# Optimization experiments

Hardware: AMD Instinct MI355X
Metric: run time of the kernel (lower is better)

## Reference

```python
import jax, jax.numpy as jnp
import numpy as np

D_MODEL = 1024
NUM_HEADS = 16
D_STATE = D_MODEL // NUM_HEADS
BS, SEQ = 8, 1024
NEG_BIG = 1e10


def setup_inputs() -> dict:
    key = jax.random.key(0)
    ks = jax.random.split(key, 3)
    std = 0.02
    x = jax.random.normal(ks[0], (BS, SEQ, D_MODEL), dtype=jnp.float32)
    qkv_w = jax.random.normal(ks[1], (D_MODEL, 3 * D_MODEL), dtype=jnp.float32) * std
    qkv_b = jnp.zeros((3 * D_MODEL,), dtype=jnp.float32)
    out_w = jax.random.normal(ks[2], (D_MODEL, D_MODEL), dtype=jnp.float32) * std
    out_b = jnp.zeros((D_MODEL,), dtype=jnp.float32)
    return {"x": x, "qkv_w": qkv_w, "qkv_b": qkv_b, "out_w": out_w, "out_b": out_b}


def reference(x, qkv_w, qkv_b, out_w, out_b):
    bs, n, d = x.shape
    qkv = jnp.matmul(x, qkv_w) + qkv_b  # [bs, n, 3*d_model]
    q, k, v = jnp.split(qkv, 3, axis=-1)

    def split_heads(t):  # [bs, n, d] -> [bs, h, n, d_state]
        return t.reshape(bs, n, NUM_HEADS, D_STATE).transpose(0, 2, 1, 3)

    q, k, v = split_heads(q), split_heads(k), split_heads(v)
    scale = 1.0 / np.sqrt(D_STATE).astype(np.float32)
    scores = jnp.einsum('bhqd,bhkd->bhqk', q, k) * scale  # [bs,h,n,n]
    # causal mask: i >= j (mask(n) with ns==nd)
    m = (jnp.arange(n)[:, None] >= jnp.arange(n)[None, :]).astype(scores.dtype)
    scores = scores * m - (1.0 - m) * NEG_BIG
    attn = jax.nn.softmax(scores, axis=-1)
    out = jnp.einsum('bhqk,bhkd->bhqd', attn, v)  # [bs,h,n,d_state]
    out = out.transpose(0, 2, 1, 3).reshape(bs, n, d)
    return jnp.matmul(out, out_w) + out_b
```

## Files before the change

kernel.cpp:

```cpp
#include <hip/hip_runtime.h>
#include <hip/hip_bf16.h>
#include <stdint.h>

typedef __attribute__((ext_vector_type(8))) __bf16 bf16x8;
typedef __attribute__((ext_vector_type(4))) float f32x4;
typedef __attribute__((ext_vector_type(4))) unsigned int u32x4;
typedef __attribute__((ext_vector_type(4))) unsigned short u16x4;

#define SEQ 1024
#define DM 1024

#if __has_builtin(__builtin_amdgcn_exp2f)
#define EXP2(x) __builtin_amdgcn_exp2f(x)
#else
#define EXP2(x) exp2f(x)
#endif

typedef __attribute__((address_space(3))) void lds_t;
typedef __attribute__((address_space(1))) void glb_t;

__device__ __forceinline__ unsigned short f2bf(float f){
  __hip_bfloat16 h = __float2bfloat16(f);
  return __builtin_bit_cast(unsigned short, h);
}
__device__ __forceinline__ bf16x8 ld16(const unsigned short* p){
  u32x4 v = *(const u32x4*)p;
  return __builtin_bit_cast(bf16x8, v);
}
__device__ __forceinline__ void gload_lds16(const unsigned short* g, unsigned short* l){
  __builtin_amdgcn_global_load_lds((const glb_t*)g, (lds_t*)l, 16, 0, 0);
}

__global__ void cvt_f32_bf16(const float* __restrict__ in,
                             unsigned short* __restrict__ out, int n)
{
  int i = (blockIdx.x * blockDim.x + threadIdx.x) * 8;
  if (i >= n) return;
  float4 a = *(const float4*)(in + i);
  float4 b = *(const float4*)(in + i + 4);
  unsigned short v[8] = { f2bf(a.x), f2bf(a.y), f2bf(a.z), f2bf(a.w),
                          f2bf(b.x), f2bf(b.y), f2bf(b.z), f2bf(b.w) };
  *(u32x4*)(out + i) = *(u32x4*)v;
}

__global__ void transpose_cvt(const float* __restrict__ in,
                              unsigned short* __restrict__ out, int R, int C)
{
  __shared__ unsigned short t[32][33];
  int x  = blockIdx.x * 32 + threadIdx.x;
  int y0 = blockIdx.y * 32 + threadIdx.y;
#pragma unroll
  for (int i = 0; i < 32; i += 8)
    t[threadIdx.y + i][threadIdx.x] = f2bf(in[(size_t)(y0 + i) * C + x]);
  __syncthreads();
  int ox  = blockIdx.y * 32 + threadIdx.x;
  int oy0 = blockIdx.x * 32 + threadIdx.y;
#pragma unroll
  for (int i = 0; i < 32; i += 8)
    out[(size_t)(oy0 + i) * R + ox] = t[threadIdx.x][threadIdx.y + i];
}

__global__ __launch_bounds__(512, 2)
void gemm_qkv(const unsigned short* __restrict__ A,
              const unsigned short* __restrict__ Bt,
              const float* __restrict__ bias,
              unsigned short* __restrict__ qko, unsigned short* __restrict__ vT,
              int M, int N, int K)
{
  __shared__ unsigned short As[4][8192];
  __shared__ unsigned short Bs[4][8192];
  const int tid = threadIdx.x;
  const int l = tid & 63;
  const int w = tid >> 6;
  const int wm = w >> 2, wn = w & 3;

  const int nbn = N >> 8;
  const int nwg = gridDim.x;
  const int bid = blockIdx.x;
  const int qq  = nwg >> 3;
  const int sb  = (bid & 7) * qq + (bid >> 3);
  const int bm = sb / nbn, bn = sb % nbn;
  const int row0 = bm << 8, col0 = bn << 8;

  const int rs = tid >> 2;
  const int cS = ((tid & 3) ^ ((tid >> 3) & 3)) * 8;
  const unsigned short* ag = A  + (size_t)(row0 + rs) * K + cS;
  const unsigned short* bg = Bt + (size_t)(col0 + rs) * K + cS;

  auto STAGE = [&](int kt, int bi) {
    const unsigned short* a = ag + kt * 32;
    const unsigned short* b = bg + kt * 32;
    gload_lds16(a,                   &As[bi][w * 512]);
    gload_lds16(a + (size_t)128 * K, &As[bi][4096 + w * 512]);
    gload_lds16(b,                   &Bs[bi][w * 512]);
    gload_lds16(b + (size_t)128 * K, &Bs[bi][4096 + w * 512]);
  };

  const f32x4 zz = {0.f, 0.f, 0.f, 0.f};
  f32x4 acc[8][4];
#pragma unroll
  for (int m = 0; m < 8; m++)
#pragma unroll
    for (int n = 0; n < 4; n++) acc[m][n] = zz;

  const int c16 = l & 15;
  const int csw = ((l >> 4) * 8) ^ (((l >> 1) & 3) << 3);
  const int NT = K >> 5;

  STAGE(0, 0);
  STAGE(1, 1);
  STAGE(2, 2);
  asm volatile("s_waitcnt vmcnt(8)" ::: "memory");
  __builtin_amdgcn_s_barrier();

  for (int t = 0; t < NT; t++) {
    const int bi = t & 3;
    if (t + 3 < NT) STAGE(t + 3, (t + 3) & 3);

    bf16x8 bfr[4], af[4];
#pragma unroll
    for (int n = 0; n < 4; n++)
      bfr[n] = ld16(&Bs[bi][(wn * 64 + n * 16 + c16) * 32 + csw]);
#pragma unroll
    for (int m = 0; m < 4; m++)
      af[m] = ld16(&As[bi][(wm * 128 + m * 16 + c16) * 32 + csw]);
#pragma unroll
    for (int m = 0; m < 4; m++)
#pragma unroll
      for (int n = 0; n < 4; n++)
        acc[m][n] = __builtin_amdgcn_mfma_f32_16x16x32_bf16(af[m], bfr[n], acc[m][n], 0, 0, 0);

    bf16x8 af2[4];
#pragma unroll
    for (int m = 0; m < 4; m++)
      af2[m] = ld16(&As[bi][(wm * 128 + (m + 4) * 16 + c16) * 32 + csw]);
#pragma unroll
    for (int m = 0; m < 4; m++)
#pragma unroll
      for (int n = 0; n < 4; n++)
        acc[m + 4][n] = __builtin_amdgcn_mfma_f32_16x16x32_bf16(af2[m], bfr[n], acc[m + 4][n], 0, 0, 0);

    if (t + 1 < NT) {
      if      (t + 3 < NT) asm volatile("s_waitcnt vmcnt(8)" ::: "memory");
      else if (t + 2 < NT) asm volatile("s_waitcnt vmcnt(4)" ::: "memory");
      else                 asm volatile("s_waitcnt vmcnt(0)" ::: "memory");
      __builtin_amdgcn_s_barrier();
    }
  }

#pragma unroll
  for (int n = 0; n < 4; n++) {
    int col = col0 + wn * 64 + n * 16 + c16;
    float bv = bias[col];
#pragma unroll
    for (int m = 0; m < 8; m++) {
      int rbase = row0 + wm * 128 + m * 16 + (l >> 4) * 4;
      if (col < 2048) {
        float sc = (col < 1024) ? 0.18033688f : 1.0f;
#pragma unroll
        for (int r = 0; r < 4; r++)
          qko[(size_t)(rbase + r) * 2048 + col] = f2bf((acc[m][n][r] + bv) * sc);
      } else {
        int bb = rbase >> 10, s0v = rbase & 1023;
        int hh = (col - 2048) >> 6, dd = (col - 2048) & 63;
        u16x4 pk;
#pragma unroll
        for (int r = 0; r < 4; r++) pk[r] = f2bf(acc[m][n][r] + bv);
        *(u16x4*)(vT + ((size_t)((bb * 16 + hh) * 64 + dd)) * 1024 + s0v) = pk;
      }
    }
  }
}

__global__ __launch_bounds__(256, 3)
void gemm_out(const unsigned short* __restrict__ A,
              const unsigned short* __restrict__ Bt,
              const float* __restrict__ bias,
              float* __restrict__ C, int M, int N, int K)
{
  __shared__ unsigned short Ls[3][2][128 * 32];
  const int tid = threadIdx.x;
  const int l = tid & 63;
  const int w = tid >> 6;

  const int nbn = N >> 7;
  const int nwg = gridDim.x;
  const int bid = blockIdx.x;
  const int qq  = nwg >> 3;
  const int sb  = (bid & 7) * qq + (bid >> 3);
  const int bm = sb / nbn, bn = sb % nbn;
  const int row0 = bm << 7, col0 = bn << 7;

  const int rA = w * 16 + (l >> 2);
  const int cS = ((l & 3) ^ ((l >> 3) & 3)) * 8;
  const unsigned short* ag = A  + (size_t)(row0 + rA) * K + cS;
  const unsigned short* bg = Bt + (size_t)(col0 + rA) * K + cS;

  auto STAGE = [&](int kt, int bi) {
    const unsigned short* a = ag + kt * 32;
    const unsigned short* b = bg + kt * 32;
    gload_lds16(a,                  &Ls[bi][0][w * 512]);
    gload_lds16(a + (size_t)64 * K, &Ls[bi][0][2048 + w * 512]);
    gload_lds16(b,                  &Ls[bi][1][w * 512]);
    gload_lds16(b + (size_t)64 * K, &Ls[bi][1][2048 + w * 512]);
  };

  const int wr = (w >> 1) * 64, wc = (w & 1) * 64;
  const f32x4 zz = {0.f, 0.f, 0.f, 0.f};
  f32x4 acc[4][4];
#pragma unroll
  for (int m = 0; m < 4; m++)
#pragma unroll
    for (int n = 0; n < 4; n++) acc[m][n] = zz;

  const int c16 = l & 15;
  const int csw = ((l >> 4) * 8) ^ (((l >> 1) & 3) << 3);

  const int NT = K >> 5;
  STAGE(0, 0);
  STAGE(1, 1);
  asm volatile("s_waitcnt vmcnt(4)" ::: "memory");
  __builtin_amdgcn_s_barrier();

  int cur = 0, stg = 2;
  for (int kt = 0; kt < NT; kt++) {
    if (kt + 2 < NT) STAGE(kt + 2, stg);

    const unsigned short* La = &Ls[cur][0][0];
    const unsigned short* Lb = &Ls[cur][1][0];
    bf16x8 af[4], bfr[4];
#pragma unroll
    for (int m = 0; m < 4; m++)
      af[m] = ld16(La + (wr + m * 16 + c16) * 32 + csw);
#pragma unroll
    for (int n = 0; n < 4; n++)
      bfr[n] = ld16(Lb + (wc + n * 16 + c16) * 32 + csw);
#pragma unroll
    for (int m = 0; m < 4; m++)
#pragma unroll
      for (int n = 0; n < 4; n++)
        acc[m][n] = __builtin_amdgcn_mfma_f32_16x16x32_bf16(af[m], bfr[n], acc[m][n], 0, 0, 0);

    if (kt + 1 < NT) {
      if (kt + 2 < NT) asm volatile("s_waitcnt vmcnt(4)" ::: "memory");
      else             asm volatile("s_waitcnt vmcnt(0)" ::: "memory");
      __builtin_amdgcn_s_barrier();
    }
    cur = (cur == 2) ? 0 : cur + 1;
    stg = (stg == 2) ? 0 : stg + 1;
  }

#pragma unroll
  for (int n = 0; n < 4; n++) {
    int col = col0 + wc + n * 16 + c16;
    float bv = bias[col];
#pragma unroll
    for (int m = 0; m < 4; m++) {
      int rbase = row0 + wr + m * 16 + (l >> 4) * 4;
#pragma unroll
      for (int r = 0; r < 4; r++)
        C[(size_t)(rbase + r) * N + col] = acc[m][n][r] + bv;
    }
  }
}

__global__ __launch_bounds__(256, 2)
void attn(const unsigned short* __restrict__ qk,
          const unsigned short* __restrict__ vT,
          unsigned short* __restrict__ ctx)
{
  __shared__ unsigned short Ksh[3][64 * 64];
  __shared__ unsigned short Ps[4][32 * 64];
  const int tid = threadIdx.x;
  const int l = tid & 63, w = tid >> 6;

  const int lin = blockIdx.x + (blockIdx.y << 2);
  const int xcd = lin & 7;
  const int j   = lin >> 3;
  const int bh  = xcd * 16 + (j & 15);
  const int bx  = j >> 4;
  const int b = bh >> 4, h = bh & 15;

  const unsigned short* qbase = qk + (size_t)b * SEQ * 2048;
  const unsigned short* kbase = qbase + 1024 + h * 64;
  const unsigned short* vbase = vT + (size_t)bh * 64 * 1024;
  unsigned short* Psw = Ps[w];
  const int d8 = (l >> 4) * 8;
  const int c16 = l & 15;
  const int r4 = (l >> 4) * 4;
  const int kvr = w * 8 + (l >> 3);
  const int cb  = (l & 7) * 16;

  const int qbA = 7 - bx, qbB = bx;
  const int q0A = qbA * 128 + w * 32, q0B = qbB * 128 + w * 32;
  const int ntA = (qbA + 1) * 2;
  const int kmaxA = (q0A + 31) >> 6, kmaxB = (q0B + 31) >> 6;

  bf16x8 qaA[2][2], qaB[2][2];
#pragma unroll
  for (int qc = 0; qc < 2; qc++)
#pragma unroll
    for (int kg = 0; kg < 2; kg++) {
      qaA[qc][kg] = ld16(qbase + (size_t)(q0A + qc * 16 + c16) * 2048
                               + h * 64 + kg * 32 + d8);
      qaB[qc][kg] = ld16(qbase + (size_t)(q0B + qc * 16 + c16) * 2048
                               + h * 64 + kg * 32 + d8);
    }

  const f32x4 zz = {0.f, 0.f, 0.f, 0.f};
  f32x4 oA[2][4], oB[2][4];
#pragma unroll
  for (int m = 0; m < 2; m++)
#pragma unroll
    for (int n = 0; n < 4; n++) { oA[m][n] = zz; oB[m][n] = zz; }
  float mA[2] = {-1e30f, -1e30f}, lA[2] = {0.f, 0.f};
  float mB[2] = {-1e30f, -1e30f}, lB[2] = {0.f, 0.f};

  auto STAGEK = [&](int t, int bufi) {
#pragma unroll
    for (int i = 0; i < 2; i++) {
      int row = i * 32 + kvr;
      int srcb = cb ^ ((row & 7) << 4);
      gload_lds16(kbase + (size_t)(t * 64 + row) * 2048 + (srcb >> 1),
                  &Ksh[bufi][i * 2048 + w * 512]);
    }
  };

  auto QK = [&](const unsigned short* Kc, bf16x8 (&qa)[2][2], f32x4 (&st)[4][2]) {
    bf16x8 kb[4];
    int bo0 = ((d8) * 2) ^ ((c16 & 7) << 4);
    int bo1 = (((32 + d8)) * 2) ^ ((c16 & 7) << 4);
#pragma unroll
    for (int mt = 0; mt < 4; mt++)
      kb[mt] = ld16(Kc + (mt * 16 + c16) * 64 + (bo0 >> 1));
#pragma unroll
    for (int mt = 0; mt < 4; mt++)
#pragma unroll
      for (int qc = 0; qc < 2; qc++)
        st[mt][qc] = __builtin_amdgcn_mfma_f32_16x16x32_bf16(kb[mt], qa[qc][0], zz, 0, 0, 0);
#pragma unroll
    for (int mt = 0; mt < 4; mt++)
      kb[mt] = ld16(Kc + (mt * 16 + c16) * 64 + (bo1 >> 1));
#pragma unroll
    for (int mt = 0; mt < 4; mt++)
#pragma unroll
      for (int qc = 0; qc < 2; qc++)
        st[mt][qc] = __builtin_amdgcn_mfma_f32_16x16x32_bf16(kb[mt], qa[qc][1], st[mt][qc], 0, 0, 0);
  };

  auto SMPV = [&](f32x4 (&st)[4][2], f32x4 (&o)[2][4], float (&mrun)[2],
                  float (&lrun)[2], int q0, int kvt,
                  bf16x8 (&vb0)[4], bf16x8 (&vb1)[4]) {
    if (kvt * 64 + 63 > q0) {
#pragma unroll
      for (int mt = 0; mt < 4; mt++)
#pragma unroll
        for (int qc = 0; qc < 2; qc++) {
          int qg = q0 + qc * 16 + c16;
#pragma unroll
          for (int r = 0; r < 4; r++) {
            int kvg = kvt * 64 + mt * 16 + r4 + r;
            if (kvg > qg) st[mt][qc][r] = -1e30f;
          }
        }
    }
    float plane[2];
#pragma unroll
    for (int qc = 0; qc < 2; qc++) {
      float mx = -1e30f;
#pragma unroll
      for (int mt = 0; mt < 4; mt++)
#pragma unroll
        for (int r = 0; r < 4; r++) mx = fmaxf(mx, st[mt][qc][r]);
      plane[qc] = mx;
    }
    int defer0 = __all(plane[0] - mrun[0] <= 11.5f);
    int defer1 = __all(plane[1] - mrun[1] <= 11.5f);
    float scq[2] = {1.f, 1.f};
#pragma unroll
    for (int qc = 0; qc < 2; qc++) {
      int defer = qc ? defer1 : defer0;
      if (!defer) {
        float mx = plane[qc];
        mx = fmaxf(mx, __shfl_xor(mx, 16));
        mx = fmaxf(mx, __shfl_xor(mx, 32));
        float mn = fmaxf(mrun[qc], mx);
        scq[qc] = EXP2(mrun[qc] - mn);
        mrun[qc] = mn;
      }
      float mn = mrun[qc];
      float rs = 0.f;
#pragma unroll
      for (int mt = 0; mt < 4; mt++)
#pragma unroll
        for (int r = 0; r < 4; r++) {
          float p = EXP2(st[mt][qc][r] - mn);
          st[mt][qc][r] = p;
          rs += p;
        }
      rs += __shfl_xor(rs, 16);
      rs += __shfl_xor(rs, 32);
      lrun[qc] = lrun[qc] * scq[qc] + rs;
    }
    if (!(defer0 && defer1)) {
#pragma unroll
      for (int m = 0; m < 2; m++)
#pragma unroll
        for (int r = 0; r < 4; r++) {
          float sc = __shfl(scq[m], (l & 48) | (r4 + r));
#pragma unroll
          for (int n = 0; n < 4; n++) o[m][n][r] *= sc;
        }
    }
#pragma unroll
    for (int qc = 0; qc < 2; qc++) {
      int rowl = qc * 16 + c16;
#pragma unroll
      for (int mt = 0; mt < 4; mt++) {
        int byteoff = ((mt * 16 + r4) * 2) ^ ((c16 & 7) << 4);
        u16x4 pk;
#pragma unroll
        for (int r = 0; r < 4; r++) pk[r] = f2bf(st[mt][qc][r]);
        *(u16x4*)(Psw + rowl * 64 + (byteoff >> 1)) = pk;
      }
    }
    bf16x8 pa[2];
    int bo0 = (d8 * 2) ^ ((c16 & 7) << 4);
    int bo1 = ((32 + d8) * 2) ^ ((c16 & 7) << 4);
#pragma unroll
    for (int m = 0; m < 2; m++)
      pa[m] = ld16(Psw + (m * 16 + c16) * 64 + (bo0 >> 1));
#pragma unroll
    for (int m = 0; m < 2; m++)
#pragma unroll
      for (int n = 0; n < 4; n++)
        o[m][n] = __builtin_amdgcn_mfma_f32_16x16x32_bf16(pa[m], vb0[n], o[m][n], 0, 0, 0);
#pragma unroll
    for (int m = 0; m < 2; m++)
      pa[m] = ld16(Psw + (m * 16 + c16) * 64 + (bo1 >> 1));
#pragma unroll
    for (int m = 0; m < 2; m++)
#pragma unroll
      for (int n = 0; n < 4; n++)
        o[m][n] = __builtin_amdgcn_mfma_f32_16x16x32_bf16(pa[m], vb1[n], o[m][n], 0, 0, 0);
  };

  STAGEK(0, 0);
  STAGEK(1, 1);
  asm volatile("s_waitcnt vmcnt(2)" ::: "memory");
  __builtin_amdgcn_s_barrier();

  int bufc = 0;
  for (int kvt = 0; kvt < ntA; kvt++) {
    const int bufn = bufc ? bufc - 1 : 2;
    const bool more = (kvt + 2 < ntA);
    if (more) STAGEK(kvt + 2, bufn);
    const unsigned short* Kc = Ksh[bufc];

    if (kvt <= kmaxA) {
      f32x4 st[4][2];
      QK(Kc, qaA, st);
      bf16x8 vb0[4], vb1[4];
#pragma unroll
      for (int n = 0; n < 4; n++) {
        vb0[n] = ld16(vbase + (size_t)(n * 16 + c16) * 1024 + kvt * 64 + d8);
        vb1[n] = ld16(vbase + (size_t)(n * 16 + c16) * 1024 + kvt * 64 + 32 + d8);
      }
      SMPV(st, oA, mA, lA, q0A, kvt, vb0, vb1);
      if (kvt <= kmaxB) {
        QK(Kc, qaB, st);
        SMPV(st, oB, mB, lB, q0B, kvt, vb0, vb1);
      }
    }

    if (more) asm volatile("s_waitcnt vmcnt(2)" ::: "memory");
    else      asm volatile("s_waitcnt vmcnt(0)" ::: "memory");
    __builtin_amdgcn_s_barrier();
    bufc = (bufc == 2) ? 0 : bufc + 1;
  }

  auto WRITE = [&](f32x4 (&o)[2][4], float (&lrun)[2], int q0) {
    float invq[2];
#pragma unroll
    for (int qc = 0; qc < 2; qc++) invq[qc] = 1.f / lrun[qc];
#pragma unroll
    for (int m = 0; m < 2; m++)
#pragma unroll
      for (int r = 0; r < 4; r++) {
        float inv = __shfl(invq[m], (l & 48) | (r4 + r));
        int qg = q0 + m * 16 + r4 + r;
#pragma unroll
        for (int n = 0; n < 4; n++) {
          int d = n * 16 + c16;
          ctx[(size_t)(b * SEQ + qg) * DM + h * 64 + d] = f2bf(o[m][n][r] * inv);
        }
      }
  };
  WRITE(oA, lA, q0A);
  WRITE(oB, lB, q0B);
}

extern "C" void kernel_launch(void* const* d_in, const int* in_sizes, int n_in,
                              void* d_out, int out_size, void* d_ws, size_t ws_size,
                              hipStream_t stream)
{
  const float* x     = (const float*)d_in[0];
  const float* qkv_w = (const float*)d_in[1];
  const float* qkv_b = (const float*)d_in[2];
  const float* out_w = (const float*)d_in[3];
  const float* out_b = (const float*)d_in[4];

  unsigned short* ws   = (unsigned short*)d_ws;
  unsigned short* xb   = ws;
  unsigned short* wqT  = xb  + (size_t)8192 * 1024;
  unsigned short* woT  = wqT + 3072 * 1024;
  unsigned short* qkb  = woT + 1024 * 1024;
  unsigned short* vTb  = qkb + (size_t)8192 * 2048;
  unsigned short* ctxb = vTb + (size_t)128 * 64 * 1024;

  hipLaunchKernelGGL(cvt_f32_bf16, dim3(8192 * 1024 / 8 / 256), dim3(256), 0, stream,
                     x, xb, 8192 * 1024);
  hipLaunchKernelGGL(transpose_cvt, dim3(3072 / 32, 1024 / 32), dim3(32, 8), 0, stream,
                     qkv_w, wqT, 1024, 3072);
  hipLaunchKernelGGL(transpose_cvt, dim3(1024 / 32, 1024 / 32), dim3(32, 8), 0, stream,
                     out_w, woT, 1024, 1024);
  hipLaunchKernelGGL(gemm_qkv, dim3(32 * 12), dim3(512), 0, stream,
                     xb, wqT, qkv_b, qkb, vTb, 8192, 3072, 1024);
  hipLaunchKernelGGL(attn, dim3(4, 128), dim3(256), 0, stream,
                     qkb, vTb, ctxb);
  hipLaunchKernelGGL(gemm_out, dim3(64 * 8), dim3(256), 0, stream,
                     ctxb, woT, out_b, (float*)d_out, 8192, 1024, 1024);
}
```

Before: 174.7 us.

## Retile QKV GEMM to 128x192 blocks with 4 waves and 3-stage pipeline

Changes the QKV projection GEMM from 256x256 tiles with 8 waves and a 4-deep LDS ring to 128x192 tiles with 4 waves (each computing 64x96) and a 3-deep ring. The grid grows from 384 to 1024 workgroups, which fills the CUs better and reduces the tail wave, and the smaller LDS footprint allows more blocks per CU. The cost is lower arithmetic intensity per tile, hence more global/LDS traffic per FLOP, and shallower prefetch depth.

Result: faster. 151.4 us (-13.3%).

```diff
diff --git a/kernel.cpp b/kernel.cpp
--- a/kernel.cpp
+++ b/kernel.cpp
@@ -60,27 +60,26 @@
     out[(size_t)(oy0 + i) * R + ox] = t[threadIdx.x][threadIdx.y + i];
 }
 
-__global__ __launch_bounds__(512, 2)
+__global__ __launch_bounds__(256, 2)
 void gemm_qkv(const unsigned short* __restrict__ A,
               const unsigned short* __restrict__ Bt,
               const float* __restrict__ bias,
               unsigned short* __restrict__ qko, unsigned short* __restrict__ vT,
               int M, int N, int K)
 {
-  __shared__ unsigned short As[4][8192];
-  __shared__ unsigned short Bs[4][8192];
+  __shared__ unsigned short As[3][128 * 32];
+  __shared__ unsigned short Bs[3][192 * 32];
   const int tid = threadIdx.x;
   const int l = tid & 63;
   const int w = tid >> 6;
-  const int wm = w >> 2, wn = w & 3;
-
-  const int nbn = N >> 8;
+
+  const int nbn = N / 192;
   const int nwg = gridDim.x;
   const int bid = blockIdx.x;
   const int qq  = nwg >> 3;
   const int sb  = (bid & 7) * qq + (bid >> 3);
   const int bm = sb / nbn, bn = sb % nbn;
-  const int row0 = bm << 8, col0 = bn << 8;
+  const int row0 = bm << 7, col0 = bn * 192;
 
   const int rs = tid >> 2;
   const int cS = ((tid & 3) ^ ((tid >> 3) & 3)) * 8;
@@ -91,70 +90,63 @@
     const unsigned short* a = ag + kt * 32;
     const unsigned short* b = bg + kt * 32;
     gload_lds16(a,                   &As[bi][w * 512]);
-    gload_lds16(a + (size_t)128 * K, &As[bi][4096 + w * 512]);
+    gload_lds16(a + (size_t)64 * K,  &As[bi][2048 + w * 512]);
     gload_lds16(b,                   &Bs[bi][w * 512]);
+    gload_lds16(b + (size_t)64 * K,  &Bs[bi][2048 + w * 512]);
     gload_lds16(b + (size_t)128 * K, &Bs[bi][4096 + w * 512]);
   };
 
+  const int wr = (w >> 1) * 64;
+  const int wc = (w & 1) * 96;
   const f32x4 zz = {0.f, 0.f, 0.f, 0.f};
-  f32x4 acc[8][4];
-#pragma unroll
-  for (int m = 0; m < 8; m++)
-#pragma unroll
-    for (int n = 0; n < 4; n++) acc[m][n] = zz;
+  f32x4 acc[4][6];
+#pragma unroll
+  for (int m = 0; m < 4; m++)
+#pragma unroll
+    for (int n = 0; n < 6; n++) acc[m][n] = zz;
 
   const int c16 = l & 15;
   const int csw = ((l >> 4) * 8) ^ (((l >> 1) & 3) << 3);
+
   const int NT = K >> 5;
-
   STAGE(0, 0);
   STAGE(1, 1);
-  STAGE(2, 2);
-  asm volatile("s_waitcnt vmcnt(8)" ::: "memory");
+  asm volatile("s_waitcnt vmcnt(5)" ::: "memory");
   __builtin_amdgcn_s_barrier();
 
-  for (int t = 0; t < NT; t++) {
-    const int bi = t & 3;
-    if (t + 3 < NT) STAGE(t + 3, (t + 3) & 3);
-
-    bf16x8 bfr[4], af[4];
-#pragma unroll
-    for (int n = 0; n < 4; n++)
-      bfr[n] = ld16(&Bs[bi][(wn * 64 + n * 16 + c16) * 32 + csw]);
+  int cur = 0, stg = 2;
+  for (int kt = 0; kt < NT; kt++) {
+    if (kt + 2 < NT) STAGE(kt + 2, stg);
+
+    bf16x8 af[4], bfr[6];
 #pragma unroll
     for (int m = 0; m < 4; m++)
-      af[m] = ld16(&As[bi][(wm * 128 + m * 16 + c16) * 32 + csw]);
+      af[m] = ld16(&As[cur][(wr + m * 16 + c16) * 32 + csw]);
+#pragma unroll
+    for (int n = 0; n < 6; n++)
+      bfr[n] = ld16(&Bs[cur][(wc + n * 16 + c16) * 32 + csw]);
 #pragma unroll
     for (int m = 0; m < 4; m++)
 #pragma unroll
-      for (int n = 0; n < 4; n++)
+      for (int n = 0; n < 6; n++)
         acc[m][n] = __builtin_amdgcn_mfma_f32_16x16x32_bf16(af[m], bfr[n], acc[m][n], 0, 0, 0);
 
-    bf16x8 af2[4];
-#pragma unroll
-    for (int m = 0; m < 4; m++)
-      af2[m] = ld16(&As[bi][(wm * 128 + (m + 4) * 16 + c16) * 32 + csw]);
-#pragma unroll
-    for (int m = 0; m < 4; m++)
-#pragma unroll
-      for (int n = 0; n < 4; n++)
-        acc[m + 4][n] = __builtin_amdgcn_mfma_f32_16x16x32_bf16(af2[m], bfr[n], acc[m + 4][n], 0, 0, 0);
-
-    if (t + 1 < NT) {
-      if      (t + 3 < NT) asm volatile("s_waitcnt vmcnt(8)" ::: "memory");
-      else if (t + 2 < NT) asm volatile("s_waitcnt vmcnt(4)" ::: "memory");
-      else                 asm volatile("s_waitcnt vmcnt(0)" ::: "memory");
+    if (kt + 1 < NT) {
+      if (kt + 2 < NT) asm volatile("s_waitcnt vmcnt(5)" ::: "memory");
+      else             asm volatile("s_waitcnt vmcnt(0)" ::: "memory");
       __builtin_amdgcn_s_barrier();
     }
+    cur = (cur == 2) ? 0 : cur + 1;
+    stg = (stg == 2) ? 0 : stg + 1;
   }
 
 #pragma unroll
-  for (int n = 0; n < 4; n++) {
-    int col = col0 + wn * 64 + n * 16 + c16;
+  for (int n = 0; n < 6; n++) {
+    int col = col0 + wc + n * 16 + c16;
     float bv = bias[col];
 #pragma unroll
-    for (int m = 0; m < 8; m++) {
-      int rbase = row0 + wm * 128 + m * 16 + (l >> 4) * 4;
+    for (int m = 0; m < 4; m++) {
+      int rbase = row0 + wr + m * 16 + (l >> 4) * 4;
       if (col < 2048) {
         float sc = (col < 1024) ? 0.18033688f : 1.0f;
 #pragma unroll
@@ -524,7 +516,7 @@
                      qkv_w, wqT, 1024, 3072);
   hipLaunchKernelGGL(transpose_cvt, dim3(1024 / 32, 1024 / 32), dim3(32, 8), 0, stream,
                      out_w, woT, 1024, 1024);
-  hipLaunchKernelGGL(gemm_qkv, dim3(32 * 12), dim3(512), 0, stream,
+  hipLaunchKernelGGL(gemm_qkv, dim3(64 * 16), dim3(256), 0, stream,
                      xb, wqT, qkv_b, qkb, vTb, 8192, 3072, 1024);
   hipLaunchKernelGGL(attn, dim3(4, 128), dim3(256), 0, stream,
                      qkb, vTb, ctxb);
```

## Interleave split A/B staging with MFMA phases using barriers and setprio in QKV GEMM

Applied to the files above, without the earlier changes.

Restructures the QKV GEMM main loop so prefetch depth drops from 3 to 2 tiles ahead. The A and B global-to-LDS loads are split and issued between the two MFMA halves, with extra barriers and s_setprio raising priority around MFMA blocks (ping-pong style scheduling). The aim is to overlap memory issue with matrix math and keep waves in lockstep. The cost is more barriers per iteration and a shallower prefetch, which may expose memory latency.

Result: faster. 160.0 us (-8.4%).

```diff
diff --git a/kernel.cpp b/kernel.cpp
--- a/kernel.cpp
+++ b/kernel.cpp
@@ -67,8 +67,8 @@
               unsigned short* __restrict__ qko, unsigned short* __restrict__ vT,
               int M, int N, int K)
 {
-  __shared__ unsigned short As[4][8192];
-  __shared__ unsigned short Bs[4][8192];
+  __shared__ unsigned short As[4][256 * 32];
+  __shared__ unsigned short Bs[4][256 * 32];
   const int tid = threadIdx.x;
   const int l = tid & 63;
   const int w = tid >> 6;
@@ -87,11 +87,13 @@
   const unsigned short* ag = A  + (size_t)(row0 + rs) * K + cS;
   const unsigned short* bg = Bt + (size_t)(col0 + rs) * K + cS;
 
-  auto STAGE = [&](int kt, int bi) {
+  auto STAGE_A = [&](int kt, int bi) {
     const unsigned short* a = ag + kt * 32;
-    const unsigned short* b = bg + kt * 32;
     gload_lds16(a,                   &As[bi][w * 512]);
     gload_lds16(a + (size_t)128 * K, &As[bi][4096 + w * 512]);
+  };
+  auto STAGE_B = [&](int kt, int bi) {
+    const unsigned short* b = bg + kt * 32;
     gload_lds16(b,                   &Bs[bi][w * 512]);
     gload_lds16(b + (size_t)128 * K, &Bs[bi][4096 + w * 512]);
   };
@@ -107,45 +109,54 @@
   const int csw = ((l >> 4) * 8) ^ (((l >> 1) & 3) << 3);
   const int NT = K >> 5;
 
-  STAGE(0, 0);
-  STAGE(1, 1);
-  STAGE(2, 2);
-  asm volatile("s_waitcnt vmcnt(8)" ::: "memory");
+  STAGE_A(0, 0); STAGE_B(0, 0);
+  STAGE_A(1, 1); STAGE_B(1, 1);
+  asm volatile("s_waitcnt vmcnt(4)" ::: "memory");
   __builtin_amdgcn_s_barrier();
 
   for (int t = 0; t < NT; t++) {
     const int bi = t & 3;
-    if (t + 3 < NT) STAGE(t + 3, (t + 3) & 3);
-
-    bf16x8 bfr[4], af[4];
+    const int si = (t + 2) & 3;
+    const bool stg = (t + 2 < NT);
+
+    bf16x8 af[4], bfr[4];
+#pragma unroll
+    for (int m = 0; m < 4; m++)
+      af[m] = ld16(&As[bi][(wm * 128 + m * 16 + c16) * 32 + csw]);
 #pragma unroll
     for (int n = 0; n < 4; n++)
       bfr[n] = ld16(&Bs[bi][(wn * 64 + n * 16 + c16) * 32 + csw]);
-#pragma unroll
-    for (int m = 0; m < 4; m++)
-      af[m] = ld16(&As[bi][(wm * 128 + m * 16 + c16) * 32 + csw]);
+    if (stg) STAGE_A(t + 2, si);
+    __builtin_amdgcn_s_barrier();
+    asm volatile("s_waitcnt lgkmcnt(0)" ::: "memory");
+    __builtin_amdgcn_s_setprio(1);
 #pragma unroll
     for (int m = 0; m < 4; m++)
 #pragma unroll
       for (int n = 0; n < 4; n++)
         acc[m][n] = __builtin_amdgcn_mfma_f32_16x16x32_bf16(af[m], bfr[n], acc[m][n], 0, 0, 0);
+    __builtin_amdgcn_s_setprio(0);
+    __builtin_amdgcn_s_barrier();
 
     bf16x8 af2[4];
 #pragma unroll
     for (int m = 0; m < 4; m++)
       af2[m] = ld16(&As[bi][(wm * 128 + (m + 4) * 16 + c16) * 32 + csw]);
+    if (stg) STAGE_B(t + 2, si);
+    __builtin_amdgcn_s_barrier();
+    asm volatile("s_waitcnt lgkmcnt(0)" ::: "memory");
+    __builtin_amdgcn_s_setprio(1);
 #pragma unroll
     for (int m = 0; m < 4; m++)
 #pragma unroll
       for (int n = 0; n < 4; n++)
         acc[m + 4][n] = __builtin_amdgcn_mfma_f32_16x16x32_bf16(af2[m], bfr[n], acc[m + 4][n], 0, 0, 0);
-
+    __builtin_amdgcn_s_setprio(0);
     if (t + 1 < NT) {
-      if      (t + 3 < NT) asm volatile("s_waitcnt vmcnt(8)" ::: "memory");
-      else if (t + 2 < NT) asm volatile("s_waitcnt vmcnt(4)" ::: "memory");
-      else                 asm volatile("s_waitcnt vmcnt(0)" ::: "memory");
-      __builtin_amdgcn_s_barrier();
-    }
+      if (stg) asm volatile("s_waitcnt vmcnt(4)" ::: "memory");
+      else     asm volatile("s_waitcnt vmcnt(0)" ::: "memory");
+    }
+    __builtin_amdgcn_s_barrier();
   }
 
 #pragma unroll
```
